# Kernel optimization log

Hardware: AMD Instinct MI355X
Metric: run time of the kernel (lower is better)

The kernel has to match this reference:

```python
import jax, jax.numpy as jnp
import numpy as np
from jax import lax

PDIM, NB, K, SK, HID = 64, 8, 13, 3, 32  # pdim, num_bases, k, sk_size, hidden=max(16,64//2)


def _mlp(pooled, w1, b1, w2, b2):
    # 1x1 convs on a 1x1 spatial map == dense layers on pooled features
    h = jax.nn.gelu(pooled @ w1.T + b1, approximate=False)
    return h @ w2.T + b2


def _depthwise_per_sample(x1, kern, pad):
    # x1: [B, pdim, H, W]; kern: [B*pdim, 1, kh, kw] -> per-sample per-channel depthwise conv
    B, C, H, W = x1.shape
    xr = x1.reshape(1, B * C, H, W)
    out = lax.conv_general_dilated(
        xr, kern, window_strides=(1, 1), padding=[(pad, pad), (pad, pad)],
        dimension_numbers=('NCHW', 'OIHW', 'NCHW'), feature_group_count=B * C)
    return out.reshape(B, C, H, W)


def setup_inputs() -> dict:
    key = jax.random.key(0)
    ks = jax.random.split(key, 16)
    B, C, H, W = 8, 96, 256, 256
    pin = PDIM
    d = {
        'x': jax.random.normal(ks[0], (B, C, H, W), jnp.float32),
        'lk_bases': jax.random.normal(ks[1], (NB, 1, K, K), jnp.float32) * 0.01,
        'router_w1': jax.random.normal(ks[2], (HID, pin), jnp.float32) * 0.05,
        'router_b1': jnp.zeros((HID,), jnp.float32),
        'router_w2': jax.random.normal(ks[3], (PDIM * NB, HID), jnp.float32) * 0.05,
        'router_b2': jnp.zeros((PDIM * NB,), jnp.float32),
        'sk_w1': jax.random.normal(ks[4], (HID, pin), jnp.float32) * 0.05,
        'sk_b1': jnp.zeros((HID,), jnp.float32),
        'sk_w2': jax.random.normal(ks[5], (PDIM * SK * SK, HID), jnp.float32) * 0.05,
        'sk_b2': jnp.zeros((PDIM * SK * SK,), jnp.float32),
        'gate_w1': jax.random.normal(ks[6], (HID, pin), jnp.float32) * 0.05,
        'gate_b1': jnp.zeros((HID,), jnp.float32),
        'gate_w2': jax.random.normal(ks[7], (PDIM * 2, HID), jnp.float32) * 0.05,
        'gate_b2': jnp.zeros((PDIM * 2,), jnp.float32),
        'fuse_w': jax.random.normal(ks[8], (PDIM, PDIM), jnp.float32) * 0.05,
        'fuse_b': jnp.zeros((PDIM,), jnp.float32),
    }
    return d


def reference(x, lk_bases, router_w1, router_b1, router_w2, router_b2,
              sk_w1, sk_b1, sk_w2, sk_b2, gate_w1, gate_b1, gate_w2, gate_b2,
              fuse_w, fuse_b):
    B, C, H, W = x.shape
    x1, x2 = x[:, :PDIM], x[:, PDIM:]
    pooled = jnp.mean(x[:, :PDIM], axis=(2, 3))  # [B, pin] (AdaptiveAvgPool2d(1))

    # router -> softmax basis weights -> composed large kernels [B, pdim, k, k]
    rw = jax.nn.softmax(_mlp(pooled, router_w1, router_b1, router_w2, router_b2)
                        .reshape(B, PDIM, NB), axis=-1)
    composed = jnp.einsum('bcn,nij->bcij', rw, lk_bases[:, 0])
    out_lk = _depthwise_per_sample(x1, composed.reshape(B * PDIM, 1, K, K), K // 2)

    # dynamic small kernels [B*pdim, 1, sk, sk]
    dyn_k = _mlp(pooled, sk_w1, sk_b1, sk_w2, sk_b2).reshape(B * PDIM, 1, SK, SK)
    out_dyn = _depthwise_per_sample(x1, dyn_k, SK // 2)

    # gated fusion (lk_filter=None branch -> out_ext = 0)
    g = jax.nn.softmax(_mlp(pooled, gate_w1, gate_b1, gate_w2, gate_b2)
                       .reshape(B, 2, PDIM), axis=1)
    g_lk = g[:, 0, :, None, None]
    g_dyn = g[:, 1, :, None, None]
    fused = g_lk * out_lk + g_dyn * out_dyn

    y1 = jnp.einsum('bchw,oc->bohw', fused, fuse_w) + fuse_b[None, :, None, None] + x1
    return jnp.concatenate([y1, x2], axis=1)
```

## Files before the change

### kernel.cpp

```cpp
#include <hip/hip_runtime.h>
#include <math.h>

#define CH 96
#define HH 256
#define WW 256
#define PD 64
#define NBASE 8
#define KK 13
#define HID 32
#define PLANE 65536

__global__ __launch_bounds__(256) void pool_kernel(const float* __restrict__ x,
                                                   float* __restrict__ partial) {
    int blk = blockIdx.x;
    int q = blk & 3, c = (blk >> 2) & 63, b = blk >> 8;
    const float4* p4 = (const float4*)(x + (size_t)(b * CH + c) * PLANE) + q * 4096;
    int t = threadIdx.x;
    float s = 0.f;
#pragma unroll
    for (int i = 0; i < 16; ++i) {
        float4 v = p4[t + (i << 8)];
        s += v.x + v.y + v.z + v.w;
    }
#pragma unroll
    for (int off = 32; off; off >>= 1) s += __shfl_down(s, off, 64);
    __shared__ float ls[4];
    if ((t & 63) == 0) ls[t >> 6] = s;
    __syncthreads();
    if (t == 0) partial[blk] = ls[0] + ls[1] + ls[2] + ls[3];
}

__global__ __launch_bounds__(256) void mlp_kernel(
    const float* __restrict__ partial, const float* __restrict__ lk_bases,
    const float* __restrict__ rw1, const float* __restrict__ rb1,
    const float* __restrict__ rw2, const float* __restrict__ rb2,
    const float* __restrict__ sw1, const float* __restrict__ sb1,
    const float* __restrict__ sw2, const float* __restrict__ sb2,
    const float* __restrict__ gw1, const float* __restrict__ gb1,
    const float* __restrict__ gw2, const float* __restrict__ gb2,
    float* __restrict__ keff) {
    int b = blockIdx.x;
    int t = threadIdx.x;
    __shared__ float pl[64];
    __shared__ float h[3][HID];
    __shared__ float ro[PD * NBASE];
    __shared__ float go[2 * PD];
    __shared__ float rw[PD][NBASE];
    __shared__ float dk_s[PD * 9];
    __shared__ float gl_s[PD], gd_s[PD];

    if (t < 64) {
        const float* pp = &partial[(b * 64 + t) * 4];
        pl[t] = (pp[0] + pp[1] + pp[2] + pp[3]) * (1.f / 65536.f);
    }
    __syncthreads();

    if (t < 96) {
        int m = t >> 5, u = t & 31;
        const float* w1 = (m == 0) ? rw1 : ((m == 1) ? sw1 : gw1);
        const float* b1 = (m == 0) ? rb1 : ((m == 1) ? sb1 : gb1);
        float a = b1[u];
#pragma unroll
        for (int i = 0; i < 64; ++i) a += w1[u * 64 + i] * pl[i];
        h[m][u] = a * 0.5f * (1.f + erff(a * 0.70710678118654752f));
    }
    __syncthreads();

    for (int o = t; o < PD * NBASE; o += 256) {
        float a = rb2[o];
#pragma unroll
        for (int i = 0; i < HID; ++i) a += rw2[o * HID + i] * h[0][i];
        ro[o] = a;
    }
    for (int o = t; o < PD * 9; o += 256) {
        float a = sb2[o];
#pragma unroll
        for (int i = 0; i < HID; ++i) a += sw2[o * HID + i] * h[1][i];
        dk_s[o] = a;
    }
    if (t < 2 * PD) {
        float a = gb2[t];
#pragma unroll
        for (int i = 0; i < HID; ++i) a += gw2[t * HID + i] * h[2][i];
        go[t] = a;
    }
    __syncthreads();

    if (t < 64) {
        float m = -1e30f;
#pragma unroll
        for (int n = 0; n < NBASE; ++n) m = fmaxf(m, ro[t * NBASE + n]);
        float e[NBASE], s = 0.f;
#pragma unroll
        for (int n = 0; n < NBASE; ++n) { e[n] = expf(ro[t * NBASE + n] - m); s += e[n]; }
        float inv = 1.f / s;
#pragma unroll
        for (int n = 0; n < NBASE; ++n) rw[t][n] = e[n] * inv;
        float a0 = go[t], a1 = go[64 + t];
        float mm = fmaxf(a0, a1);
        float e0 = expf(a0 - mm), e1 = expf(a1 - mm);
        float gi = 1.f / (e0 + e1);
        gl_s[t] = e0 * gi;
        gd_s[t] = e1 * gi;
    }
    __syncthreads();

    for (int idx = t; idx < 64 * 169; idx += 256) {
        int c = idx / 169;
        int tap = idx - c * 169;
        int dy = tap / 13, dx = tap - dy * 13;
        float a = 0.f;
#pragma unroll
        for (int n = 0; n < NBASE; ++n) a += rw[c][n] * lk_bases[n * 169 + tap];
        a *= gl_s[c];
        if (dy >= 5 && dy < 8 && dx >= 5 && dx < 8)
            a += gd_s[c] * dk_s[c * 9 + (dy - 5) * 3 + (dx - 5)];
        keff[(size_t)(b * 64 + c) * 169 + tap] = a;
    }
}

#define TDIM 64
#define TSTR 76
#define TROWS 76

__global__ __launch_bounds__(256) void conv_kernel(
    const float* __restrict__ x, const float* __restrict__ keff,
    float* __restrict__ outp) {
    int tx = blockIdx.x;
    int wt = tx & 3, ht = tx >> 2;
    int c = blockIdx.y, b = blockIdx.z;
    int h0 = ht * TDIM, w0 = wt * TDIM;
    int t = threadIdx.x;

    __shared__ __align__(16) float tile[TROWS * TSTR];

    const float* xp = x + (size_t)(b * CH + c) * PLANE;
    for (int idx = t; idx < TROWS * TSTR; idx += 256) {
        int rr = idx / TSTR, cc = idx - rr * TSTR;
        int gh = h0 - 6 + rr, gw = w0 - 6 + cc;
        float v = 0.f;
        if (gh >= 0 && gh < HH && gw >= 0 && gw < WW) v = xp[gh * WW + gw];
        tile[idx] = v;
    }
    __syncthreads();

    const float* krow = keff + (size_t)(b * 64 + c) * 169;

    int tc = t & 15;
    int tr = t >> 4;

    float acc[4][4] = {{0.f}};
    float kw[4][13];

#pragma unroll
    for (int j = 0; j < 16; ++j) {
        const float* xr = &tile[(4 * tr + j) * TSTR + 4 * tc];
        float xv[16];
        *(float4*)&xv[0]  = *(const float4*)&xr[0];
        *(float4*)&xv[4]  = *(const float4*)&xr[4];
        *(float4*)&xv[8]  = *(const float4*)&xr[8];
        *(float4*)&xv[12] = *(const float4*)&xr[12];
        if (j < 13) {
#pragma unroll
            for (int d = 0; d < 13; ++d) kw[j & 3][d] = krow[j * 13 + d];
        }
#pragma unroll
        for (int i = 0; i < 4; ++i) {
            const int dy = j - i;
            if (dy >= 0 && dy < 13) {
#pragma unroll
                for (int dx = 0; dx < 13; ++dx)
#pragma unroll
                    for (int m = 0; m < 4; ++m)
                        acc[i][m] = fmaf(kw[dy & 3][dx], xv[dx + m], acc[i][m]);
            }
        }
    }

    float* op = outp + (size_t)(b * CH + c) * PLANE + (size_t)(h0 + 4 * tr) * WW + (w0 + 4 * tc);
#pragma unroll
    for (int i = 0; i < 4; ++i)
        *(float4*)&op[(size_t)i * WW] = *(float4*)&acc[i][0];
}

__global__ __launch_bounds__(256) void pwcopy_kernel(
    const float* __restrict__ x, const float* __restrict__ fw,
    const float* __restrict__ fb, float* outp) {
    int b = blockIdx.y;
    int px = blockIdx.x * 256 + threadIdx.x;
    const size_t bb = (size_t)b * CH * PLANE;

    float f[64];
#pragma unroll
    for (int c = 0; c < 64; ++c) f[c] = outp[bb + (size_t)c * PLANE + px];

    for (int o = 0; o < 64; ++o) {
        float a = fb[o];
#pragma unroll
        for (int c2 = 0; c2 < 64; ++c2) a = fmaf(fw[o * 64 + c2], f[c2], a);
        outp[bb + (size_t)o * PLANE + px] = a + x[bb + (size_t)o * PLANE + px];
    }
#pragma unroll
    for (int c = 0; c < 32; ++c) {
        size_t off = bb + (size_t)(64 + c) * PLANE + px;
        outp[off] = x[off];
    }
}

extern "C" void kernel_launch(void* const* d_in, const int* in_sizes, int n_in,
                              void* d_out, int out_size, void* d_ws, size_t ws_size,
                              hipStream_t stream) {
    const float* x        = (const float*)d_in[0];
    const float* lk_bases = (const float*)d_in[1];
    const float* rw1      = (const float*)d_in[2];
    const float* rb1      = (const float*)d_in[3];
    const float* rw2      = (const float*)d_in[4];
    const float* rb2      = (const float*)d_in[5];
    const float* sw1      = (const float*)d_in[6];
    const float* sb1      = (const float*)d_in[7];
    const float* sw2      = (const float*)d_in[8];
    const float* sb2      = (const float*)d_in[9];
    const float* gw1      = (const float*)d_in[10];
    const float* gb1      = (const float*)d_in[11];
    const float* gw2      = (const float*)d_in[12];
    const float* gb2      = (const float*)d_in[13];
    const float* fw       = (const float*)d_in[14];
    const float* fb       = (const float*)d_in[15];
    float* outp = (float*)d_out;

    float* wsf     = (float*)d_ws;
    float* partial = wsf;
    float* keff    = wsf + 2048;

    pool_kernel<<<dim3(2048), dim3(256), 0, stream>>>(x, partial);
    mlp_kernel<<<dim3(8), dim3(256), 0, stream>>>(partial, lk_bases,
        rw1, rb1, rw2, rb2, sw1, sb1, sw2, sb2, gw1, gb1, gw2, gb2, keff);
    conv_kernel<<<dim3(16, 64, 8), dim3(256), 0, stream>>>(x, keff, outp);
    pwcopy_kernel<<<dim3(256, 8), dim3(256), 0, stream>>>(x, fw, fb, outp);
}
```

Before: 385.5 us.

## Store fused conv output as bf16 and run pointwise fuse on MFMA

The depthwise conv now writes its fused output as bf16 into the x2 region of the output buffer, halving intermediate traffic. The 64x64 pointwise fuse uses bf16 MFMA 16x16x32 instructions instead of scalar FMAs over 64 registers per thread. The x2 passthrough copy moves into a separate vectorized kernel that runs afterwards and overwrites the scratch area. This lowers precision of both the intermediate and the fuse weights to bf16, and the bf16 intermediate is read with strided 2-byte loads.

```diff
diff --git a/kernel.cpp b/kernel.cpp
--- a/kernel.cpp
+++ b/kernel.cpp
@@ -9,6 +9,15 @@
 #define KK 13
 #define HID 32
 #define PLANE 65536
+
+typedef float f32x4 __attribute__((ext_vector_type(4)));
+typedef short s16x8 __attribute__((ext_vector_type(8)));
+
+__device__ inline ushort f2bf(float f) {
+    uint u = __float_as_uint(f);
+    u += 0x7fff + ((u >> 16) & 1);
+    return (ushort)(u >> 16);
+}
 
 __global__ __launch_bounds__(256) void pool_kernel(const float* __restrict__ x,
                                                    float* __restrict__ partial) {
@@ -177,34 +186,82 @@
         }
     }
 
-    float* op = outp + (size_t)(b * CH + c) * PLANE + (size_t)(h0 + 4 * tr) * WW + (w0 + 4 * tc);
-#pragma unroll
-    for (int i = 0; i < 4; ++i)
-        *(float4*)&op[(size_t)i * WW] = *(float4*)&acc[i][0];
-}
-
-__global__ __launch_bounds__(256) void pwcopy_kernel(
+    ushort* fB = (ushort*)(outp + ((size_t)b * CH + 64) * PLANE);
+    size_t base = (size_t)c * PLANE + (size_t)(h0 + 4 * tr) * WW + (w0 + 4 * tc);
+#pragma unroll
+    for (int i = 0; i < 4; ++i) {
+        uint2 u;
+        u.x = (uint)f2bf(acc[i][0]) | ((uint)f2bf(acc[i][1]) << 16);
+        u.y = (uint)f2bf(acc[i][2]) | ((uint)f2bf(acc[i][3]) << 16);
+        *(uint2*)&fB[base + (size_t)i * WW] = u;
+    }
+}
+
+__global__ __launch_bounds__(256) void pw_kernel(
     const float* __restrict__ x, const float* __restrict__ fw,
     const float* __restrict__ fb, float* outp) {
     int b = blockIdx.y;
-    int px = blockIdx.x * 256 + threadIdx.x;
+    int w = threadIdx.x >> 6;
+    int l = threadIdx.x & 63;
+    int px0 = blockIdx.x * 256 + w * 64;
+    int lr = l & 15;
+    int lg = l >> 4;
+
+    const ushort* fBS = (const ushort*)(outp + ((size_t)b * CH + 64) * PLANE);
     const size_t bb = (size_t)b * CH * PLANE;
 
-    float f[64];
-#pragma unroll
-    for (int c = 0; c < 64; ++c) f[c] = outp[bb + (size_t)c * PLANE + px];
-
-    for (int o = 0; o < 64; ++o) {
-        float a = fb[o];
-#pragma unroll
-        for (int c2 = 0; c2 < 64; ++c2) a = fmaf(fw[o * 64 + c2], f[c2], a);
-        outp[bb + (size_t)o * PLANE + px] = a + x[bb + (size_t)o * PLANE + px];
-    }
-#pragma unroll
-    for (int c = 0; c < 32; ++c) {
-        size_t off = bb + (size_t)(64 + c) * PLANE + px;
-        outp[off] = x[off];
-    }
+    s16x8 wa[4][2];
+#pragma unroll
+    for (int ot = 0; ot < 4; ++ot)
+#pragma unroll
+        for (int ks = 0; ks < 2; ++ks) {
+            const float* src = fw + (ot * 16 + lr) * 64 + ks * 32 + lg * 8;
+            float4 a0 = *(const float4*)(src);
+            float4 a1 = *(const float4*)(src + 4);
+            s16x8 v;
+            v[0] = (short)f2bf(a0.x); v[1] = (short)f2bf(a0.y);
+            v[2] = (short)f2bf(a0.z); v[3] = (short)f2bf(a0.w);
+            v[4] = (short)f2bf(a1.x); v[5] = (short)f2bf(a1.y);
+            v[6] = (short)f2bf(a1.z); v[7] = (short)f2bf(a1.w);
+            wa[ot][ks] = v;
+        }
+
+#pragma unroll
+    for (int pxg = 0; pxg < 4; ++pxg) {
+        int px = px0 + pxg * 16 + lr;
+        s16x8 vb[2];
+#pragma unroll
+        for (int ks = 0; ks < 2; ++ks) {
+            const ushort* src = fBS + (size_t)(ks * 32 + lg * 8) * PLANE + px;
+            s16x8 v;
+#pragma unroll
+            for (int i = 0; i < 8; ++i) v[i] = (short)src[(size_t)i * PLANE];
+            vb[ks] = v;
+        }
+#pragma unroll
+        for (int ot = 0; ot < 4; ++ot) {
+            f32x4 acc = {0.f, 0.f, 0.f, 0.f};
+            acc = __builtin_amdgcn_mfma_f32_16x16x32_bf16(wa[ot][0], vb[0], acc, 0, 0, 0);
+            acc = __builtin_amdgcn_mfma_f32_16x16x32_bf16(wa[ot][1], vb[1], acc, 0, 0, 0);
+            float4 fbv = *(const float4*)(fb + ot * 16 + lg * 4);
+#pragma unroll
+            for (int i = 0; i < 4; ++i) {
+                int o = ot * 16 + lg * 4 + i;
+                size_t off = bb + (size_t)o * PLANE + px;
+                outp[off] = acc[i] + ((const float*)&fbv)[i] + x[off];
+            }
+        }
+    }
+}
+
+__global__ __launch_bounds__(256) void copy_kernel(const float* __restrict__ x,
+                                                   float* __restrict__ outp) {
+    size_t i = (size_t)blockIdx.x * 256 + threadIdx.x;
+    int b = (int)(i >> 19);
+    size_t off = i & 524287;
+    const float4* s = (const float4*)(x + ((size_t)b * CH + 64) * PLANE) + off;
+    float4* d = (float4*)(outp + ((size_t)b * CH + 64) * PLANE) + off;
+    *d = *s;
 }
 
 extern "C" void kernel_launch(void* const* d_in, const int* in_sizes, int n_in,
@@ -236,5 +293,6 @@
     mlp_kernel<<<dim3(8), dim3(256), 0, stream>>>(partial, lk_bases,
         rw1, rb1, rw2, rb2, sw1, sb1, sw2, sb2, gw1, gb1, gw2, gb2, keff);
     conv_kernel<<<dim3(16, 64, 8), dim3(256), 0, stream>>>(x, keff, outp);
-    pwcopy_kernel<<<dim3(256, 8), dim3(256), 0, stream>>>(x, fw, fb, outp);
-}
+    pw_kernel<<<dim3(256, 8), dim3(256), 0, stream>>>(x, fw, fb, outp);
+    copy_kernel<<<dim3(16384), dim3(256), 0, stream>>>(x, outp);
+}
```

After: 361.4 us. -6.2%, faster.
